# Kernel optimization log

Hardware: AMD Instinct MI355X
Metric: run time of the kernel (lower is better)

## Reference

```python
import jax, jax.numpy as jnp
import numpy as np
import math

H, D, DFF = 12, 768, 3072
DH = D // H  # 64
B, T = 4, 2048
EPS = 1e-5


def setup_inputs() -> dict:
    key = jax.random.key(0)
    ks = jax.random.split(key, 12)
    randw = lambda k, *d: jax.random.normal(k, d, jnp.float32) / math.sqrt(d[-1])
    return {
        "X": jax.random.normal(ks[0], (B, T, D), jnp.float32),
        "w_q": randw(ks[1], H, DH, D),
        "w_k": randw(ks[2], H, DH, D),
        "w_v": randw(ks[3], H, DH, D),
        "w_o": randw(ks[4], DH * H, D),
        "W1": jax.random.normal(ks[5], (DFF, D), jnp.float32) * 0.02,
        "b1": jnp.zeros((DFF,), jnp.float32),
        "W2": jax.random.normal(ks[6], (D, DFF), jnp.float32) * 0.02,
        "b2": jnp.zeros((D,), jnp.float32),
        "g1": jnp.ones((D,), jnp.float32),
        "be1": jnp.zeros((D,), jnp.float32),
        "g2": jnp.ones((D,), jnp.float32),
        "be2": jnp.zeros((D,), jnp.float32),
    }


def layernorm(x, g, b):
    mu = jnp.mean(x, axis=-1, keepdims=True)
    var = jnp.var(x, axis=-1, keepdims=True)
    return (x - mu) * jax.lax.rsqrt(var + EPS) * g + b


def attention(x, w_q, w_k, w_v, w_o):
    # x: [n,t,c]
    q = jnp.einsum('ntc,hdc->nhtd', x, w_q)
    k = jnp.einsum('ntc,hdc->nhtd', x, w_k)
    v = jnp.einsum('ntc,hdc->nhtd', x, w_v)
    a = jnp.einsum('nhtd,nhsd->nhts', q, k) / math.sqrt(q.shape[3])
    t, s = a.shape[2], a.shape[3]
    forbidden = jnp.arange(t)[:, None] < jnp.arange(s)[None, :]
    a = jnp.where(forbidden, -jnp.inf, a)
    a = jax.nn.softmax(a, axis=3)
    y = jnp.einsum('nhts,nhsd->nthd', a, v).reshape(x.shape[0], t, -1)
    return y @ w_o


def reference(X, w_q, w_k, w_v, w_o, W1, b1, W2, b2, g1, be1, g2, be2):
    X = X + attention(layernorm(X, g1, be1), w_q, w_k, w_v, w_o)
    h = jax.nn.relu(layernorm(X, g2, be2) @ W1.T + b1)
    return X + h @ W2.T + b2
```

## Files before the change

### kernel.cpp

```cpp
#include <hip/hip_runtime.h>
#include <stdint.h>

#define B_   4
#define T_   2048
#define D_   768
#define H_   12
#define DH_  64
#define DFF_ 3072
#define NTOK_ (B_*T_)
#define QKVN_ (3*D_)

typedef unsigned short u16;
typedef unsigned int u32;
typedef __bf16 bf16x8 __attribute__((ext_vector_type(8)));
typedef float  f32x4  __attribute__((ext_vector_type(4)));

__device__ __forceinline__ u16 f2bf(float f) {
  union { float f; unsigned u; } v; v.f = f;
  return (u16)((v.u + 0x7fffu + ((v.u >> 16) & 1u)) >> 16);
}

__device__ __forceinline__ u32 pack_bf2(float a, float b) {
  union { float f; u32 u; } ua, ub; ua.f = a; ub.f = b;
  return ((ua.u + 0x8000u) >> 16) | ((ub.u + 0x8000u) & 0xFFFF0000u);
}

__device__ __forceinline__ float fast_exp2(float x) {
#if __has_builtin(__builtin_amdgcn_exp2f)
  return __builtin_amdgcn_exp2f(x);
#else
  return exp2f(x);
#endif
}

__device__ __forceinline__ float fast_rcp(float x) {
#if __has_builtin(__builtin_amdgcn_rcpf)
  return __builtin_amdgcn_rcpf(x);
#else
  return 1.0f / x;
#endif
}

__device__ __forceinline__ void gload_lds16(const void* g, void* l) {
  __builtin_amdgcn_global_load_lds(
      (__attribute__((address_space(1))) unsigned int*)(void*)g,
      (__attribute__((address_space(3))) unsigned int*)l, 16, 0, 0);
}

template<bool BIAS, bool RELU, bool RES, bool BF16OUT, bool QSCALE, int BN,
         bool VTRANS>
__global__ __launch_bounds__(256) void gemm_bt(
    const u16* __restrict__ A, const u16* __restrict__ Bw,
    const float* __restrict__ bias, const float* __restrict__ res,
    void* __restrict__ outp, u16* __restrict__ vtp, int M, int N, int K)
{
  constexpr int NI = BN / 32;
  __shared__ u16 lA[2 * 128 * 32];
  __shared__ u16 lB[2 * BN * 32];
  const int tid  = threadIdx.x;
  const int lane = tid & 63;
  const int wave = tid >> 6;
  const int quad = lane >> 4;
  const int l15  = lane & 15;
  const int mBase = blockIdx.x * 128;
  const int nBase = blockIdx.y * BN;
  const int wm = (wave >> 1) * 64;
  const int wn = (wave & 1) * (BN / 2);

  const f32x4 fz = {0.f, 0.f, 0.f, 0.f};
  f32x4 acc[4][NI];
#pragma unroll
  for (int i = 0; i < 4; i++)
#pragma unroll
    for (int j = 0; j < NI; j++) acc[i][j] = fz;

  const int c0 = tid, c1 = tid + 256;
  const u16* gA0 = A  + (size_t)(mBase + (c0 >> 2)) * K + (c0 & 3) * 8;
  const u16* gA1 = A  + (size_t)(mBase + (c1 >> 2)) * K + (c1 & 3) * 8;
  const u16* gB0 = Bw + (size_t)(nBase + (c0 >> 2)) * K + (c0 & 3) * 8;
  const u16* gB1 = (BN == 128)
      ? Bw + (size_t)(nBase + (c1 >> 2)) * K + (c1 & 3) * 8 : nullptr;
  u16* lA0 = lA + c0 * 8; u16* lA1 = lA + c1 * 8;
  u16* lB0 = lB + c0 * 8;
  u16* lB1 = (BN == 128) ? lB + c1 * 8 : nullptr;

  for (int kt = 0; kt < K; kt += 64) {
    gload_lds16(gA0 + kt,      lA0);
    gload_lds16(gA1 + kt,      lA1);
    gload_lds16(gA0 + kt + 32, lA0 + 128 * 32);
    gload_lds16(gA1 + kt + 32, lA1 + 128 * 32);
    gload_lds16(gB0 + kt,      lB0);
    gload_lds16(gB0 + kt + 32, lB0 + BN * 32);
    if (BN == 128) {
      gload_lds16(gB1 + kt,      lB1);
      gload_lds16(gB1 + kt + 32, lB1 + BN * 32);
    }
    __syncthreads();
#pragma unroll
    for (int hf = 0; hf < 2; hf++) {
      const u16* lAh = lA + hf * (128 * 32);
      const u16* lBh = lB + hf * (BN * 32);
      bf16x8 af[4], bfr[NI];
#pragma unroll
      for (int mi = 0; mi < 4; mi++)
        af[mi] = *(const bf16x8*)(lAh + (wm + mi * 16 + l15) * 32 + quad * 8);
#pragma unroll
      for (int ni = 0; ni < NI; ni++)
        bfr[ni] = *(const bf16x8*)(lBh + (wn + ni * 16 + l15) * 32 + quad * 8);
#pragma unroll
      for (int mi = 0; mi < 4; mi++)
#pragma unroll
        for (int ni = 0; ni < NI; ni++)
          acc[mi][ni] = __builtin_amdgcn_mfma_f32_16x16x32_bf16(
              af[mi], bfr[ni], acc[mi][ni], 0, 0, 0);
    }
    __syncthreads();
  }

#pragma unroll
  for (int mi = 0; mi < 4; mi++) {
#pragma unroll
    for (int ni = 0; ni < NI; ni++) {
      const int col = nBase + wn + ni * 16 + l15;
      if (VTRANS && col >= 2 * D_) {
        const int n  = col - 2 * D_;
        const int hh = n >> 6, dd = n & 63;
        const int row0 = mBase + wm + mi * 16 + quad * 4;
        const int bb = row0 >> 11, tt = row0 & (T_ - 1);
        ushort4 pk;
        pk.x = f2bf(acc[mi][ni][0]); pk.y = f2bf(acc[mi][ni][1]);
        pk.z = f2bf(acc[mi][ni][2]); pk.w = f2bf(acc[mi][ni][3]);
        *(ushort4*)(vtp + ((size_t)((bb * H_ + hh) * DH_ + dd)) * T_ + tt) = pk;
        continue;
      }
      float bv = 0.f;
      if (BIAS) bv = bias[col];
#pragma unroll
      for (int r = 0; r < 4; r++) {
        const int row = mBase + wm + mi * 16 + quad * 4 + r;
        float v = acc[mi][ni][r];
        if (BIAS) v += bv;
        if (RELU) v = fmaxf(v, 0.f);
        if (RES)  v += res[(size_t)row * N + col];
        if (QSCALE && col < D_) v *= 0.180336880f;
        if (BF16OUT) ((u16*)outp)[(size_t)row * N + col] = f2bf(v);
        else        ((float*)outp)[(size_t)row * N + col] = v;
      }
    }
  }
}

__global__ __launch_bounds__(256) void attn_kernel(
    const u16* __restrict__ qkv, const u16* __restrict__ vt, u16* __restrict__ Y)
{
  __shared__ u16 lK[2][64 * 64];
  __shared__ u16 lV[2][64 * 64];
  __shared__ u32 lP[4][2 * 16 * 36];
  const int tid  = threadIdx.x;
  const int lane = tid & 63;
  const int wave = tid >> 6;
  const int quad = lane >> 4;
  const int l15  = lane & 15;
  const int pi = (int)blockIdx.x;
  const int h  = blockIdx.y;
  const int b  = blockIdx.z;
  const int qw0 = (wave < 2) ? (pi * 64 + wave * 32)
                             : ((31 - pi) * 64 + (wave - 2) * 32);

  bf16x8 qA0, qA1, qB0, qB1;
  {
    const u16* qp = qkv + (size_t)(b * T_ + qw0 + l15) * QKVN_ + h * DH_ + quad * 8;
    qA0 = *(const bf16x8*)(qp);
    qA1 = *(const bf16x8*)(qp + 32);
    const u16* qp2 = qp + 16 * QKVN_;
    qB0 = *(const bf16x8*)(qp2);
    qB1 = *(const bf16x8*)(qp2 + 32);
  }

  const f32x4 fz = {0.f, 0.f, 0.f, 0.f};
  f32x4 oA[4], oB[4];
#pragma unroll
  for (int i = 0; i < 4; i++) { oA[i] = fz; oB[i] = fz; }
  float lsA = 0.f, lsB = 0.f;

  const int c0 = tid, c1 = tid + 256;
  const int r0 = c0 >> 3, j0 = (c0 & 7) ^ (r0 & 7);
  const int r1 = c1 >> 3, j1 = (c1 & 7) ^ (r1 & 7);
  const u16* gK0 = qkv + (size_t)(b * T_ + r0) * QKVN_ + D_ + h * DH_ + j0 * 8;
  const u16* gK1 = qkv + (size_t)(b * T_ + r1) * QKVN_ + D_ + h * DH_ + j1 * 8;
  const u16* gV0 = vt + (size_t)((b * H_ + h) * DH_ + r0) * T_ + j0 * 8;
  const u16* gV1 = vt + (size_t)((b * H_ + h) * DH_ + r1) * T_ + j1 * 8;

  const int njs = 32 - pi;

  gload_lds16(gK0, lK[0] + c0 * 8);
  gload_lds16(gK1, lK[0] + c1 * 8);
  gload_lds16(gV0, lV[0] + c0 * 8);
  gload_lds16(gV1, lV[0] + c1 * 8);

  u32* lpA = &lP[wave][0];
  u32* lpB = &lP[wave][576];
  const int wbase = l15 * 36 + quad * 2;
  const int rb0   = l15 * 36 + quad * 4;

  for (int js = 0; js < njs; js++) {
    const int cur = js & 1;
    __syncthreads();

    if (js + 1 < njs) {
      const size_t s1 = (size_t)(js + 1) * 64;
      const int nb = cur ^ 1;
      gload_lds16(gK0 + s1 * QKVN_, lK[nb] + c0 * 8);
      gload_lds16(gK1 + s1 * QKVN_, lK[nb] + c1 * 8);
      gload_lds16(gV0 + s1,         lV[nb] + c0 * 8);
      gload_lds16(gV1 + s1,         lV[nb] + c1 * 8);
    }

    const int s0 = js * 64;
    if (s0 > qw0 + 31) continue;

    const u16* lKc = lK[cur];
    const u16* lVc = lV[cur];

    f32x4 sA[4], sB[4];
#pragma unroll
    for (int ni = 0; ni < 4; ni++) {
      const int row = ni * 16 + l15;
      const int sw = row & 7;
      const bf16x8 k0 = *(const bf16x8*)(lKc + row * 64 + ((quad ^ sw) * 8));
      const bf16x8 k1 = *(const bf16x8*)(lKc + row * 64 + (((4 + quad) ^ sw) * 8));
      f32x4 tA = fz, tB = fz;
      tA = __builtin_amdgcn_mfma_f32_16x16x32_bf16(k0, qA0, tA, 0, 0, 0);
      tA = __builtin_amdgcn_mfma_f32_16x16x32_bf16(k1, qA1, tA, 0, 0, 0);
      tB = __builtin_amdgcn_mfma_f32_16x16x32_bf16(k0, qB0, tB, 0, 0, 0);
      tB = __builtin_amdgcn_mfma_f32_16x16x32_bf16(k1, qB1, tB, 0, 0, 0);
      sA[ni] = tA; sB[ni] = tB;
    }

    const bool nm = (s0 + 63 > qw0);
    const int qA_idx = qw0 + l15;
    const int qB_idx = qA_idx + 16;
#pragma unroll
    for (int ni = 0; ni < 4; ni++) {
      const int sbase = s0 + ni * 16 + quad * 4;
      float pa[4], pb[4];
#pragma unroll
      for (int r = 0; r < 4; r++) {
        float va = fast_exp2(sA[ni][r]);
        float vb = fast_exp2(sB[ni][r]);
        if (nm) {
          if (sbase + r > qA_idx) va = 0.f;
          if (sbase + r > qB_idx) vb = 0.f;
        }
        pa[r] = va; pb[r] = vb;
        lsA += va; lsB += vb;
      }
      lpA[wbase + ni * 8 + 0] = pack_bf2(pa[0], pa[1]);
      lpA[wbase + ni * 8 + 1] = pack_bf2(pa[2], pa[3]);
      lpB[wbase + ni * 8 + 0] = pack_bf2(pb[0], pb[1]);
      lpB[wbase + ni * 8 + 1] = pack_bf2(pb[2], pb[3]);
    }
    __asm__ volatile("s_waitcnt lgkmcnt(0)" ::: "memory");

    const bf16x8 pA0 = *(const bf16x8*)(lpA + rb0);
    const bf16x8 pA1 = *(const bf16x8*)(lpA + rb0 + 16);
    const bf16x8 pB0 = *(const bf16x8*)(lpB + rb0);
    const bf16x8 pB1 = *(const bf16x8*)(lpB + rb0 + 16);

#pragma unroll
    for (int dt = 0; dt < 4; dt++) {
      const int row = dt * 16 + l15;
      const int sw = row & 7;
      const bf16x8 v0 = *(const bf16x8*)(lVc + row * 64 + ((quad ^ sw) * 8));
      const bf16x8 v1 = *(const bf16x8*)(lVc + row * 64 + (((4 + quad) ^ sw) * 8));
      oA[dt] = __builtin_amdgcn_mfma_f32_16x16x32_bf16(v0, pA0, oA[dt], 0, 0, 0);
      oA[dt] = __builtin_amdgcn_mfma_f32_16x16x32_bf16(v1, pA1, oA[dt], 0, 0, 0);
      oB[dt] = __builtin_amdgcn_mfma_f32_16x16x32_bf16(v0, pB0, oB[dt], 0, 0, 0);
      oB[dt] = __builtin_amdgcn_mfma_f32_16x16x32_bf16(v1, pB1, oB[dt], 0, 0, 0);
    }
  }

  lsA += __shfl_xor(lsA, 16); lsA += __shfl_xor(lsA, 32);
  lsB += __shfl_xor(lsB, 16); lsB += __shfl_xor(lsB, 32);
  const float rlA = fast_rcp(lsA);
  const float rlB = fast_rcp(lsB);

#pragma unroll
  for (int dt = 0; dt < 4; dt++) {
    const int dbase = h * DH_ + dt * 16 + quad * 4;
    ushort4 pa, pb;
    pa.x = f2bf(oA[dt][0] * rlA); pa.y = f2bf(oA[dt][1] * rlA);
    pa.z = f2bf(oA[dt][2] * rlA); pa.w = f2bf(oA[dt][3] * rlA);
    pb.x = f2bf(oB[dt][0] * rlB); pb.y = f2bf(oB[dt][1] * rlB);
    pb.z = f2bf(oB[dt][2] * rlB); pb.w = f2bf(oB[dt][3] * rlB);
    *(ushort4*)(Y + (size_t)(b * T_ + qw0 + l15) * D_ + dbase) = pa;
    *(ushort4*)(Y + (size_t)(b * T_ + qw0 + 16 + l15) * D_ + dbase) = pb;
  }
}

__device__ __forceinline__ void ln_row(
    const float* __restrict__ X, const float* __restrict__ g,
    const float* __restrict__ be, u16* __restrict__ out, int row)
{
  const float* x = X + (size_t)row * D_;
  const int t = threadIdx.x;
  const float v0 = x[t], v1 = x[t + 256], v2 = x[t + 512];
  float s = v0 + v1 + v2;
  float sq = v0 * v0 + v1 * v1 + v2 * v2;
#pragma unroll
  for (int off = 1; off < 64; off <<= 1) {
    s  += __shfl_xor(s, off);
    sq += __shfl_xor(sq, off);
  }
  __shared__ float ws_[4], wq_[4];
  const int wv = t >> 6, lane = t & 63;
  if (lane == 0) { ws_[wv] = s; wq_[wv] = sq; }
  __syncthreads();
  s  = ws_[0] + ws_[1] + ws_[2] + ws_[3];
  sq = wq_[0] + wq_[1] + wq_[2] + wq_[3];
  const float mean = s * (1.f / 768.f);
  const float var  = sq * (1.f / 768.f) - mean * mean;
  const float rstd = rsqrtf(var + 1e-5f);
  u16* o = out + (size_t)row * D_;
  int c = t;
  o[c] = f2bf((v0 - mean) * rstd * g[c] + be[c]); c += 256;
  o[c] = f2bf((v1 - mean) * rstd * g[c] + be[c]); c += 256;
  o[c] = f2bf((v2 - mean) * rstd * g[c] + be[c]);
}

__global__ __launch_bounds__(256) void ln_kernel(
    const float* __restrict__ X, const float* __restrict__ g,
    const float* __restrict__ be, u16* __restrict__ out)
{
  ln_row(X, g, be, out, blockIdx.x);
}

__global__ __launch_bounds__(256) void prep_kernel(
    const float* __restrict__ X, const float* __restrict__ g1,
    const float* __restrict__ be1, u16* __restrict__ xln,
    const float* __restrict__ w_q, const float* __restrict__ w_k,
    const float* __restrict__ w_v, const float* __restrict__ W1,
    const float* __restrict__ W2, const float* __restrict__ w_o,
    u16* __restrict__ wqkv, u16* __restrict__ W1b,
    u16* __restrict__ W2b, u16* __restrict__ woT)
{
  if (blockIdx.x < NTOK_) {
    ln_row(X, g1, be1, xln, blockIdx.x);
    return;
  }
  const int id = blockIdx.x - NTOK_;
  if (id < 144) {
    __shared__ float tile[64][65];
    const int bx = id % 12, by = id / 12;
    const int rr0 = by * 64, cc0 = bx * 64;
    for (int idx = threadIdx.x; idx < 4096; idx += 256) {
      const int i = idx >> 6, j = idx & 63;
      tile[i][j] = w_o[(size_t)(rr0 + i) * D_ + cc0 + j];
    }
    __syncthreads();
    for (int idx = threadIdx.x; idx < 4096; idx += 256) {
      const int i = idx >> 6, j = idx & 63;
      woT[(size_t)(cc0 + i) * D_ + rr0 + j] = f2bf(tile[j][i]);
    }
  } else {
    const int WQN = H_ * DH_ * D_;
    const int i = (id - 144) * 256 + threadIdx.x;
    if (i < 3 * WQN) {
      const float* src = (i < WQN) ? w_q : (i < 2 * WQN ? w_k : w_v);
      const int off = (i < WQN) ? i : (i < 2 * WQN ? i - WQN : i - 2 * WQN);
      wqkv[i] = f2bf(src[off]);
    } else if (i < 3 * WQN + DFF_ * D_) {
      const int off = i - 3 * WQN;
      W1b[off] = f2bf(W1[off]);
    } else {
      const int off = i - 3 * WQN - DFF_ * D_;
      W2b[off] = f2bf(W2[off]);
    }
  }
}

extern "C" void kernel_launch(void* const* d_in, const int* in_sizes, int n_in,
                              void* d_out, int out_size, void* d_ws, size_t ws_size,
                              hipStream_t stream) {
  const float* X   = (const float*)d_in[0];
  const float* w_q = (const float*)d_in[1];
  const float* w_k = (const float*)d_in[2];
  const float* w_v = (const float*)d_in[3];
  const float* w_o = (const float*)d_in[4];
  const float* W1  = (const float*)d_in[5];
  const float* b1  = (const float*)d_in[6];
  const float* W2  = (const float*)d_in[7];
  const float* b2  = (const float*)d_in[8];
  const float* g1  = (const float*)d_in[9];
  const float* be1 = (const float*)d_in[10];
  const float* g2  = (const float*)d_in[11];
  const float* be2 = (const float*)d_in[12];
  float* out = (float*)d_out;

  char* ws = (char*)d_ws;
  u16*   qkv  = (u16*)(ws + 0);
  u16*   vt   = (u16*)(ws + 37748736);
  u16*   hbuf = (u16*)(ws + 0);
  u16*   xln  = (u16*)(ws + 50331648);
  u16*   Ybuf = (u16*)(ws + 62914560);
  float* X1   = (float*)(ws + 75497472);
  u16*   wqkv = (u16*)(ws + 100663296);
  u16*   woT  = (u16*)(ws + 104202240);
  u16*   W1b  = (u16*)(ws + 105381888);
  u16*   W2b  = (u16*)(ws + 110100480);

  prep_kernel<<<NTOK_ + 25488, 256, 0, stream>>>(
      X, g1, be1, xln, w_q, w_k, w_v, W1, W2, w_o, wqkv, W1b, W2b, woT);

  gemm_bt<false, false, false, true, true, 128, true>
      <<<dim3(64, 18), 256, 0, stream>>>(
      xln, wqkv, nullptr, nullptr, qkv, vt, NTOK_, QKVN_, D_);

  attn_kernel<<<dim3(16, 12, 4), 256, 0, stream>>>(qkv, vt, Ybuf);

  gemm_bt<false, false, true, false, false, 64, false>
      <<<dim3(64, 12), 256, 0, stream>>>(
      Ybuf, woT, nullptr, X, X1, nullptr, NTOK_, D_, D_);

  ln_kernel<<<NTOK_, 256, 0, stream>>>(X1, g2, be2, xln);

  gemm_bt<true, true, false, true, false, 128, false>
      <<<dim3(64, 24), 256, 0, stream>>>(
      xln, W1b, b1, nullptr, hbuf, nullptr, NTOK_, DFF_, D_);

  gemm_bt<true, false, true, false, false, 64, false>
      <<<dim3(64, 12), 256, 0, stream>>>(
      hbuf, W2b, b2, X1, out, nullptr, NTOK_, D_, DFF_);
}
```

Before: 370.2 us.

## Rebalance causal attention so all waves process both query tiles sequentially

Each block previously split its four waves between a low and a high query tile, leaving the low-tile waves idle for most KV iterations. Now every wave owns 16 rows of each tile and the block streams the high tile's KV range followed by the low tile's range. This is meant to remove idle waves under the causal mask. In exchange it adds extra KV tile loads and barriers and halves Q reuse per loaded K/V tile.

After: 365.1 us. Within noise of the previous version (-1.4%).

```diff
diff --git a/kernel.cpp b/kernel.cpp
--- a/kernel.cpp
+++ b/kernel.cpp
@@ -150,12 +150,64 @@
   }
 }
 
+__device__ __forceinline__ void attn_round(
+    const u16* __restrict__ lKc, const u16* __restrict__ lVc,
+    int s0, int qw0, int quad, int l15,
+    const bf16x8& q0, const bf16x8& q1,
+    f32x4 (&o)[4], float& ls, u32* __restrict__ lp, int wbase, int rb0)
+{
+  const f32x4 fz = {0.f, 0.f, 0.f, 0.f};
+  f32x4 s[4];
+#pragma unroll
+  for (int ni = 0; ni < 4; ni++) {
+    const int row = ni * 16 + l15;
+    const int sw = row & 7;
+    const bf16x8 k0 = *(const bf16x8*)(lKc + row * 64 + ((quad ^ sw) * 8));
+    const bf16x8 k1 = *(const bf16x8*)(lKc + row * 64 + (((4 + quad) ^ sw) * 8));
+    f32x4 t = fz;
+    t = __builtin_amdgcn_mfma_f32_16x16x32_bf16(k0, q0, t, 0, 0, 0);
+    t = __builtin_amdgcn_mfma_f32_16x16x32_bf16(k1, q1, t, 0, 0, 0);
+    s[ni] = t;
+  }
+
+  const bool nm = (s0 + 63 > qw0);
+  const int qidx = qw0 + l15;
+#pragma unroll
+  for (int ni = 0; ni < 4; ni++) {
+    const int sbase = s0 + ni * 16 + quad * 4;
+    float p[4];
+#pragma unroll
+    for (int r = 0; r < 4; r++) {
+      float v = fast_exp2(s[ni][r]);
+      if (nm && (sbase + r > qidx)) v = 0.f;
+      p[r] = v;
+      ls += v;
+    }
+    lp[wbase + ni * 8 + 0] = pack_bf2(p[0], p[1]);
+    lp[wbase + ni * 8 + 1] = pack_bf2(p[2], p[3]);
+  }
+  __asm__ volatile("s_waitcnt lgkmcnt(0)" ::: "memory");
+
+  const bf16x8 p0 = *(const bf16x8*)(lp + rb0);
+  const bf16x8 p1 = *(const bf16x8*)(lp + rb0 + 16);
+
+#pragma unroll
+  for (int dt = 0; dt < 4; dt++) {
+    const int row = dt * 16 + l15;
+    const int sw = row & 7;
+    const bf16x8 v0 = *(const bf16x8*)(lVc + row * 64 + ((quad ^ sw) * 8));
+    const bf16x8 v1 = *(const bf16x8*)(lVc + row * 64 + (((4 + quad) ^ sw) * 8));
+    o[dt] = __builtin_amdgcn_mfma_f32_16x16x32_bf16(v0, p0, o[dt], 0, 0, 0);
+    o[dt] = __builtin_amdgcn_mfma_f32_16x16x32_bf16(v1, p1, o[dt], 0, 0, 0);
+  }
+}
+
 __global__ __launch_bounds__(256) void attn_kernel(
     const u16* __restrict__ qkv, const u16* __restrict__ vt, u16* __restrict__ Y)
 {
   __shared__ u16 lK[2][64 * 64];
   __shared__ u16 lV[2][64 * 64];
-  __shared__ u32 lP[4][2 * 16 * 36];
+  __shared__ u32 lP[4][16 * 36];
   const int tid  = threadIdx.x;
   const int lane = tid & 63;
   const int wave = tid >> 6;
@@ -164,24 +216,27 @@
   const int pi = (int)blockIdx.x;
   const int h  = blockIdx.y;
   const int b  = blockIdx.z;
-  const int qw0 = (wave < 2) ? (pi * 64 + wave * 32)
-                             : ((31 - pi) * 64 + (wave - 2) * 32);
-
-  bf16x8 qA0, qA1, qB0, qB1;
+  const int tH = 31 - pi, tL = pi;
+  const int njsH = tH + 1;
+  const int total = njsH + tL + 1;
+  const int qwH = tH * 64 + wave * 16;
+  const int qwL = tL * 64 + wave * 16;
+
+  bf16x8 qH0, qH1, qL0, qL1;
   {
-    const u16* qp = qkv + (size_t)(b * T_ + qw0 + l15) * QKVN_ + h * DH_ + quad * 8;
-    qA0 = *(const bf16x8*)(qp);
-    qA1 = *(const bf16x8*)(qp + 32);
-    const u16* qp2 = qp + 16 * QKVN_;
-    qB0 = *(const bf16x8*)(qp2);
-    qB1 = *(const bf16x8*)(qp2 + 32);
+    const u16* qp = qkv + (size_t)(b * T_ + qwH + l15) * QKVN_ + h * DH_ + quad * 8;
+    qH0 = *(const bf16x8*)(qp);
+    qH1 = *(const bf16x8*)(qp + 32);
+    const u16* qp2 = qkv + (size_t)(b * T_ + qwL + l15) * QKVN_ + h * DH_ + quad * 8;
+    qL0 = *(const bf16x8*)(qp2);
+    qL1 = *(const bf16x8*)(qp2 + 32);
   }
 
   const f32x4 fz = {0.f, 0.f, 0.f, 0.f};
-  f32x4 oA[4], oB[4];
-#pragma unroll
-  for (int i = 0; i < 4; i++) { oA[i] = fz; oB[i] = fz; }
-  float lsA = 0.f, lsB = 0.f;
+  f32x4 oH[4], oL[4];
+#pragma unroll
+  for (int i = 0; i < 4; i++) { oH[i] = fz; oL[i] = fz; }
+  float lsH = 0.f, lsL = 0.f;
 
   const int c0 = tid, c1 = tid + 256;
   const int r0 = c0 >> 3, j0 = (c0 & 7) ^ (r0 & 7);
@@ -191,24 +246,22 @@
   const u16* gV0 = vt + (size_t)((b * H_ + h) * DH_ + r0) * T_ + j0 * 8;
   const u16* gV1 = vt + (size_t)((b * H_ + h) * DH_ + r1) * T_ + j1 * 8;
 
-  const int njs = 32 - pi;
-
   gload_lds16(gK0, lK[0] + c0 * 8);
   gload_lds16(gK1, lK[0] + c1 * 8);
   gload_lds16(gV0, lV[0] + c0 * 8);
   gload_lds16(gV1, lV[0] + c1 * 8);
 
-  u32* lpA = &lP[wave][0];
-  u32* lpB = &lP[wave][576];
+  u32* lp = &lP[wave][0];
   const int wbase = l15 * 36 + quad * 2;
   const int rb0   = l15 * 36 + quad * 4;
 
-  for (int js = 0; js < njs; js++) {
-    const int cur = js & 1;
+  for (int i = 0; i < total; i++) {
+    const int cur = i & 1;
     __syncthreads();
 
-    if (js + 1 < njs) {
-      const size_t s1 = (size_t)(js + 1) * 64;
+    if (i + 1 < total) {
+      const int sn = (i + 1 < njsH) ? (i + 1) : (i + 1 - njsH);
+      const size_t s1 = (size_t)sn * 64;
       const int nb = cur ^ 1;
       gload_lds16(gK0 + s1 * QKVN_, lK[nb] + c0 * 8);
       gload_lds16(gK1 + s1 * QKVN_, lK[nb] + c1 * 8);
@@ -216,85 +269,32 @@
       gload_lds16(gV1 + s1,         lV[nb] + c1 * 8);
     }
 
-    const int s0 = js * 64;
-    if (s0 > qw0 + 31) continue;
-
     const u16* lKc = lK[cur];
     const u16* lVc = lV[cur];
-
-    f32x4 sA[4], sB[4];
-#pragma unroll
-    for (int ni = 0; ni < 4; ni++) {
-      const int row = ni * 16 + l15;
-      const int sw = row & 7;
-      const bf16x8 k0 = *(const bf16x8*)(lKc + row * 64 + ((quad ^ sw) * 8));
-      const bf16x8 k1 = *(const bf16x8*)(lKc + row * 64 + (((4 + quad) ^ sw) * 8));
-      f32x4 tA = fz, tB = fz;
-      tA = __builtin_amdgcn_mfma_f32_16x16x32_bf16(k0, qA0, tA, 0, 0, 0);
-      tA = __builtin_amdgcn_mfma_f32_16x16x32_bf16(k1, qA1, tA, 0, 0, 0);
-      tB = __builtin_amdgcn_mfma_f32_16x16x32_bf16(k0, qB0, tB, 0, 0, 0);
-      tB = __builtin_amdgcn_mfma_f32_16x16x32_bf16(k1, qB1, tB, 0, 0, 0);
-      sA[ni] = tA; sB[ni] = tB;
-    }
-
-    const bool nm = (s0 + 63 > qw0);
-    const int qA_idx = qw0 + l15;
-    const int qB_idx = qA_idx + 16;
-#pragma unroll
-    for (int ni = 0; ni < 4; ni++) {
-      const int sbase = s0 + ni * 16 + quad * 4;
-      float pa[4], pb[4];
-#pragma unroll
-      for (int r = 0; r < 4; r++) {
-        float va = fast_exp2(sA[ni][r]);
-        float vb = fast_exp2(sB[ni][r]);
-        if (nm) {
-          if (sbase + r > qA_idx) va = 0.f;
-          if (sbase + r > qB_idx) vb = 0.f;
-        }
-        pa[r] = va; pb[r] = vb;
-        lsA += va; lsB += vb;
-      }
-      lpA[wbase + ni * 8 + 0] = pack_bf2(pa[0], pa[1]);
-      lpA[wbase + ni * 8 + 1] = pack_bf2(pa[2], pa[3]);
-      lpB[wbase + ni * 8 + 0] = pack_bf2(pb[0], pb[1]);
-      lpB[wbase + ni * 8 + 1] = pack_bf2(pb[2], pb[3]);
-    }
-    __asm__ volatile("s_waitcnt lgkmcnt(0)" ::: "memory");
-
-    const bf16x8 pA0 = *(const bf16x8*)(lpA + rb0);
-    const bf16x8 pA1 = *(const bf16x8*)(lpA + rb0 + 16);
-    const bf16x8 pB0 = *(const bf16x8*)(lpB + rb0);
-    const bf16x8 pB1 = *(const bf16x8*)(lpB + rb0 + 16);
-
-#pragma unroll
-    for (int dt = 0; dt < 4; dt++) {
-      const int row = dt * 16 + l15;
-      const int sw = row & 7;
-      const bf16x8 v0 = *(const bf16x8*)(lVc + row * 64 + ((quad ^ sw) * 8));
-      const bf16x8 v1 = *(const bf16x8*)(lVc + row * 64 + (((4 + quad) ^ sw) * 8));
-      oA[dt] = __builtin_amdgcn_mfma_f32_16x16x32_bf16(v0, pA0, oA[dt], 0, 0, 0);
-      oA[dt] = __builtin_amdgcn_mfma_f32_16x16x32_bf16(v1, pA1, oA[dt], 0, 0, 0);
-      oB[dt] = __builtin_amdgcn_mfma_f32_16x16x32_bf16(v0, pB0, oB[dt], 0, 0, 0);
-      oB[dt] = __builtin_amdgcn_mfma_f32_16x16x32_bf16(v1, pB1, oB[dt], 0, 0, 0);
-    }
-  }
-
-  lsA += __shfl_xor(lsA, 16); lsA += __shfl_xor(lsA, 32);
-  lsB += __shfl_xor(lsB, 16); lsB += __shfl_xor(lsB, 32);
-  const float rlA = fast_rcp(lsA);
-  const float rlB = fast_rcp(lsB);
+    if (i < njsH) {
+      attn_round(lKc, lVc, i * 64, qwH, quad, l15, qH0, qH1, oH, lsH,
+                 lp, wbase, rb0);
+    } else {
+      attn_round(lKc, lVc, (i - njsH) * 64, qwL, quad, l15, qL0, qL1, oL, lsL,
+                 lp, wbase, rb0);
+    }
+  }
+
+  lsH += __shfl_xor(lsH, 16); lsH += __shfl_xor(lsH, 32);
+  lsL += __shfl_xor(lsL, 16); lsL += __shfl_xor(lsL, 32);
+  const float rlH = fast_rcp(lsH);
+  const float rlL = fast_rcp(lsL);
 
 #pragma unroll
   for (int dt = 0; dt < 4; dt++) {
     const int dbase = h * DH_ + dt * 16 + quad * 4;
     ushort4 pa, pb;
-    pa.x = f2bf(oA[dt][0] * rlA); pa.y = f2bf(oA[dt][1] * rlA);
-    pa.z = f2bf(oA[dt][2] * rlA); pa.w = f2bf(oA[dt][3] * rlA);
-    pb.x = f2bf(oB[dt][0] * rlB); pb.y = f2bf(oB[dt][1] * rlB);
-    pb.z = f2bf(oB[dt][2] * rlB); pb.w = f2bf(oB[dt][3] * rlB);
-    *(ushort4*)(Y + (size_t)(b * T_ + qw0 + l15) * D_ + dbase) = pa;
-    *(ushort4*)(Y + (size_t)(b * T_ + qw0 + 16 + l15) * D_ + dbase) = pb;
+    pa.x = f2bf(oH[dt][0] * rlH); pa.y = f2bf(oH[dt][1] * rlH);
+    pa.z = f2bf(oH[dt][2] * rlH); pa.w = f2bf(oH[dt][3] * rlH);
+    pb.x = f2bf(oL[dt][0] * rlL); pb.y = f2bf(oL[dt][1] * rlL);
+    pb.z = f2bf(oL[dt][2] * rlL); pb.w = f2bf(oL[dt][3] * rlL);
+    *(ushort4*)(Y + (size_t)(b * T_ + qwH + l15) * D_ + dbase) = pa;
+    *(ushort4*)(Y + (size_t)(b * T_ + qwL + l15) * D_ + dbase) = pb;
   }
 }
 
```
